# Kernel tuning notes

Measured on AMD Instinct MI355X. Metric: run time of the kernel, lower is better.

Reference implementation:

```python
import jax, jax.numpy as jnp
import numpy as np

K = 10
ALPHA = 0.1
N_NODES = 100000
N_EDGES = 5000000
HID = 16


def setup_inputs() -> dict:
    key = jax.random.key(0)
    ks = jax.random.split(key, 8)
    x = jax.random.normal(ks[0], (N_NODES, 1), dtype=jnp.float32)
    edge_index = jax.random.randint(ks[1], (2, N_EDGES), 0, N_NODES, dtype=jnp.int64)
    s = 1.0 / np.sqrt(HID)
    W1 = jax.random.normal(ks[2], (1, HID), dtype=jnp.float32)
    b1 = jax.random.normal(ks[3], (HID,), dtype=jnp.float32) * s
    W2 = jax.random.normal(ks[4], (HID, HID), dtype=jnp.float32) * s
    b2 = jax.random.normal(ks[5], (HID,), dtype=jnp.float32) * s
    W3 = jax.random.normal(ks[6], (HID, 1), dtype=jnp.float32) * s
    b3 = jax.random.normal(ks[7], (1,), dtype=jnp.float32) * s
    return {"x": x, "edge_index": edge_index, "W1": W1, "b1": b1,
            "W2": W2, "b2": b2, "W3": W3, "b3": b3}


def reference(x, edge_index, W1, b1, W2, b2, W3, b3):
    N = x.shape[0]
    # GCN normalization with self-loops (PyG APPNP default):
    # A_hat = D^{-1/2} (A + I) D^{-1/2}
    loop = jnp.arange(N, dtype=edge_index.dtype)
    src = jnp.concatenate([edge_index[0], loop])  # [E + N]
    dst = jnp.concatenate([edge_index[1], loop])
    ones = jnp.ones(src.shape[0], dtype=x.dtype)
    deg = jax.ops.segment_sum(ones, dst, num_segments=N)  # in-degree + 1
    dinv = jnp.where(deg > 0, jax.lax.rsqrt(deg), 0.0)
    norm = dinv[src] * dinv[dst]  # [E + N]

    # MLP encoder
    h = jax.nn.relu(x @ W1 + b1)
    h = jax.nn.relu(h @ W2 + b2)

    # APPNP propagation: h <- (1-alpha) * A_hat h + alpha * h0
    h0 = h
    for _ in range(K):
        msg = h[src] * norm[:, None]                         # gather + scale
        agg = jax.ops.segment_sum(msg, dst, num_segments=N)  # scatter-add
        h = (1.0 - ALPHA) * agg + ALPHA * h0

    return h @ W3 + b3
```

## Files before the change

kernel.cpp:

```cpp
#include <hip/hip_runtime.h>
#include <math.h>

#define HID 16
#define NBUCK 8
#define NSTRIPE 64
#define SLICE 11264
#define PAD 32
#define BW 12500
#define BSTEP 12500

typedef int int4v __attribute__((ext_vector_type(4)));

__global__ void partition_edges(const int* __restrict__ src, const int* __restrict__ dst,
                                int* __restrict__ scur, int* __restrict__ pairs, int E) {
    int lane = threadIdx.x & 63;
    int wib = threadIdx.x >> 6;
    int base = (blockIdx.x * 4 + wib) * 512;
    int stripe = blockIdx.x & (NSTRIPE - 1);
    unsigned long long lt = ((unsigned long long)1 << lane) - 1;

    int pk[8], bk[8], off[8];
    int wcnt[NBUCK];
#pragma unroll
    for (int b = 0; b < NBUCK; ++b) wcnt[b] = 0;

#pragma unroll
    for (int i = 0; i < 8; ++i) {
        int e = base + i * 64 + lane;
        bool valid = e < E;
        int d = valid ? dst[e] : 0;
        int s = valid ? src[e] : 0;
        int b = d / BSTEP;
        bk[i] = valid ? b : -1;
        pk[i] = ((d - b * BSTEP) << 17) | s;
#pragma unroll
        for (int bb = 0; bb < NBUCK; ++bb) {
            unsigned long long m = __ballot(valid && (b == bb));
            if (valid && b == bb) off[i] = wcnt[bb] + __popcll(m & lt);
            wcnt[bb] += __popcll(m);
        }
    }
    __shared__ int wc[4][NBUCK];
    __shared__ int wbase[4][NBUCK];
    int myc = 0;
#pragma unroll
    for (int b = 0; b < NBUCK; ++b) if (lane == b) myc = wcnt[b];
    if (lane < NBUCK) wc[wib][lane] = myc;
    __syncthreads();
    if (wib == 0 && lane < NBUCK) {
        int t0 = wc[0][lane], t1 = wc[1][lane], t2 = wc[2][lane], t3 = wc[3][lane];
        int tot = t0 + t1 + t2 + t3;
        int bb = (tot > 0) ? atomicAdd(&scur[lane * NSTRIPE + stripe], tot) : 0;
        wbase[0][lane] = bb;
        wbase[1][lane] = bb + t0;
        wbase[2][lane] = bb + t0 + t1;
        wbase[3][lane] = bb + t0 + t1 + t2;
    }
    __syncthreads();
    int mybase = (lane < NBUCK) ? wbase[wib][lane] : 0;
#pragma unroll
    for (int i = 0; i < 8; ++i) {
        if (bk[i] >= 0) {
            int b = bk[i];
            int bs = __shfl(mybase, b, 64);
            int idx = bs + off[i];
            if (idx < SLICE)
                pairs[((size_t)(b * NSTRIPE + stripe)) * SLICE + idx] = pk[i];
        }
    }
}

__global__ void count_slices(const int* __restrict__ pairs, const int* __restrict__ scur,
                             unsigned short* __restrict__ pcnt) {
    __shared__ int lcnt[BW];
    int sl = blockIdx.x;
    for (int i = threadIdx.x; i < BW; i += blockDim.x) lcnt[i] = 0;
    __syncthreads();
    int n = scur[sl];
    if (n > SLICE) n = SLICE;
    const int* seg = pairs + (size_t)sl * SLICE;
    int n4 = n >> 2;
    const int4v* seg4 = (const int4v*)seg;
    for (int q = threadIdx.x; q < n4; q += blockDim.x) {
        int4v p = seg4[q];
        atomicAdd(&lcnt[p.x >> 17], 1);
        atomicAdd(&lcnt[p.y >> 17], 1);
        atomicAdd(&lcnt[p.z >> 17], 1);
        atomicAdd(&lcnt[p.w >> 17], 1);
    }
    for (int k = (n4 << 2) + threadIdx.x; k < n; k += blockDim.x)
        atomicAdd(&lcnt[seg[k] >> 17], 1);
    __syncthreads();
    unsigned short* out = pcnt + (size_t)sl * BW;
    for (int i = threadIdx.x; i < BW; i += blockDim.x)
        out[i] = (unsigned short)lcnt[i];
}

__global__ void block_reduce(const unsigned short* __restrict__ pcnt,
                             int* __restrict__ bsum, int N) {
    int i = blockIdx.x * blockDim.x + threadIdx.x;
    int c = 0;
    if (i < N) {
        int b = i / BW;
        int loc = i - b * BW;
#pragma unroll 8
        for (int s = 0; s < NSTRIPE; ++s)
            c += pcnt[(size_t)(b * NSTRIPE + s) * BW + loc];
    }
    int v = (i < N) ? ((c + (PAD - 1)) & ~(PAD - 1)) : 0;
#pragma unroll
    for (int o = 1; o < 64; o <<= 1) v += __shfl_xor(v, o);
    __shared__ int ws[4];
    int lane = threadIdx.x & 63;
    int wid = threadIdx.x >> 6;
    if (lane == 0) ws[wid] = v;
    __syncthreads();
    if (threadIdx.x == 0) bsum[blockIdx.x] = ws[0] + ws[1] + ws[2] + ws[3];
}

__global__ void scan_bsums(int* __restrict__ bsum, int* __restrict__ row_ptr,
                           int nb, int N) {
    __shared__ int s[1024];
    int t = threadIdx.x;
    int v = (t < nb) ? bsum[t] : 0;
    s[t] = v;
    __syncthreads();
    for (int o = 1; o < 1024; o <<= 1) {
        int add = (t >= o) ? s[t - o] : 0;
        __syncthreads();
        s[t] += add;
        __syncthreads();
    }
    if (t < nb) bsum[t] = s[t] - v;
    if (t == 0) row_ptr[N] = s[1023];
}

__global__ void finalize_encode(const unsigned short* __restrict__ pcnt,
                                const int* __restrict__ bsum,
                                int* __restrict__ row_ptr, int* __restrict__ ppos,
                                float* __restrict__ w9, float* __restrict__ dinv,
                                const float* __restrict__ x, const float* __restrict__ W1,
                                const float* __restrict__ b1, const float* __restrict__ W2,
                                const float* __restrict__ b2, const float* __restrict__ W3,
                                float* __restrict__ z0, float* __restrict__ zA,
                                float* __restrict__ zB, int* __restrict__ col, int N) {
    __shared__ int sm[256];
    int t = threadIdx.x;
    int i = blockIdx.x * blockDim.x + t;
    int b = 0, loc = 0, c = 0;
    if (i < N) {
        b = i / BW;
        loc = i - b * BW;
#pragma unroll 8
        for (int s = 0; s < NSTRIPE; ++s)
            c += pcnt[(size_t)(b * NSTRIPE + s) * BW + loc];
    }
    int pc = (c + (PAD - 1)) & ~(PAD - 1);
    sm[t] = (i < N) ? pc : 0;
    __syncthreads();
    for (int o = 1; o < 256; o <<= 1) {
        int add = (t >= o) ? sm[t - o] : 0;
        __syncthreads();
        sm[t] += add;
        __syncthreads();
    }
    if (i >= N) return;
    int off = bsum[blockIdx.x] + sm[t] - pc;
    row_ptr[i] = off;
    int run = off;
#pragma unroll 8
    for (int s = 0; s < NSTRIPE; ++s) {
        ppos[(size_t)(b * NSTRIPE + s) * BW + loc] = run;
        run += pcnt[(size_t)(b * NSTRIPE + s) * BW + loc];
    }
    if (i == 0) { z0[N] = 0.0f; zA[N] = 0.0f; zB[N] = 0.0f; }
    for (int k = off + c; k < off + pc; ++k) col[k] = N;
    float deg = (float)(c + 1);
    w9[i]   = 0.9f / deg;
    float dv = rsqrtf(deg);
    dinv[i] = dv;

    float xv = x[i];
    float h1[HID];
#pragma unroll
    for (int j = 0; j < HID; ++j) h1[j] = fmaxf(xv * W1[j] + b1[j], 0.0f);
    float zacc = 0.0f;
#pragma unroll
    for (int j = 0; j < HID; ++j) {
        float acc = b2[j];
#pragma unroll
        for (int q = 0; q < HID; ++q) acc += h1[q] * W2[q * HID + j];
        zacc += fmaxf(acc, 0.0f) * W3[j];
    }
    z0[i] = dv * zacc;
}

__global__ void fill_csr3(const int* __restrict__ pairs, const int* __restrict__ scur,
                          const int* __restrict__ ppos, int* __restrict__ col) {
    __shared__ int lcur[BW];
    int b = blockIdx.x & 7;
    int s = blockIdx.x >> 3;
    int sl = b * NSTRIPE + s;
    const int* pb = ppos + (size_t)sl * BW;
    for (int i = threadIdx.x; i < BW; i += blockDim.x) lcur[i] = pb[i];
    __syncthreads();
    int n = scur[sl];
    if (n > SLICE) n = SLICE;
    const int* seg = pairs + (size_t)sl * SLICE;
    for (int k = threadIdx.x; k < n; k += blockDim.x) {
        int p = seg[k];
        int pos = atomicAdd(&lcur[p >> 17], 1);
        col[pos] = p & 0x1FFFF;
    }
}

__global__ void pack_col(const int* __restrict__ col, const int* __restrict__ row_ptr,
                         unsigned short* __restrict__ collo,
                         unsigned long long* __restrict__ colmask, int N) {
    int t = blockIdx.x * blockDim.x + threadIdx.x;
    int base = t << 6;
    if (base >= row_ptr[N]) return;
    unsigned long long m = 0;
#pragma unroll
    for (int q = 0; q < 16; ++q) {
        int4v c = *(const int4v*)(col + base + q * 4);
        unsigned long long w = (unsigned long long)(c.x & 0xFFFF)
                             | ((unsigned long long)(c.y & 0xFFFF) << 16)
                             | ((unsigned long long)(c.z & 0xFFFF) << 32)
                             | ((unsigned long long)(c.w & 0xFFFF) << 48);
        *(unsigned long long*)(collo + base + q * 4) = w;
        m |= ((unsigned long long)((c.x >> 16) & 1)) << (q * 4 + 0);
        m |= ((unsigned long long)((c.y >> 16) & 1)) << (q * 4 + 1);
        m |= ((unsigned long long)((c.z >> 16) & 1)) << (q * 4 + 2);
        m |= ((unsigned long long)((c.w >> 16) & 1)) << (q * 4 + 3);
    }
    colmask[t] = m;
}

__device__ __forceinline__ float row_sum16(const float* __restrict__ zin,
                                           const unsigned short* __restrict__ collo,
                                           const unsigned long long* __restrict__ colmask,
                                           int s, int pe, int j) {
    float a0 = 0.f, a1 = 0.f;
    for (int k = s + j * 2; k < pe; k += 32) {
        unsigned int w = *(const unsigned int*)(collo + k);
        unsigned int bits = (unsigned int)((colmask[k >> 6] >> (k & 63)) & 3ULL);
        int c0 = (int)(w & 0xFFFF)  | ((bits & 1) << 16);
        int c1 = (int)(w >> 16)     | ((bits & 2) << 15);
        a0 += zin[c0];
        a1 += zin[c1];
    }
    float acc = a0 + a1;
    acc += __shfl_xor(acc, 1, 16);
    acc += __shfl_xor(acc, 2, 16);
    acc += __shfl_xor(acc, 4, 16);
    acc += __shfl_xor(acc, 8, 16);
    return acc;
}

__device__ __forceinline__ int pin_node(int blockId, int tid) {
    int bucket = blockId & 7;
    int idx = blockId >> 3;
    return bucket * BW + idx * 16 + (tid >> 4);
}

__global__ void prop_scalar(const float* __restrict__ zin, const float* __restrict__ z0,
                            const int* __restrict__ row_ptr,
                            const unsigned short* __restrict__ collo,
                            const unsigned long long* __restrict__ colmask,
                            const float* __restrict__ w9, float* __restrict__ zout, int N) {
    int v = pin_node(blockIdx.x, threadIdx.x);
    if (v >= N) return;
    int j = threadIdx.x & 15;
    int s = row_ptr[v];
    int pe = row_ptr[v + 1];
    float acc = row_sum16(zin, collo, colmask, s, pe, j);
    if (j == 0) zout[v] = w9[v] * (acc + zin[v]) + 0.1f * z0[v];
}

__global__ void prop_last(const float* __restrict__ zin, const float* __restrict__ z0,
                          const int* __restrict__ row_ptr,
                          const unsigned short* __restrict__ collo,
                          const unsigned long long* __restrict__ colmask,
                          const float* __restrict__ w9, const float* __restrict__ dinv,
                          const float* __restrict__ b3, float* __restrict__ y, int N) {
    int v = pin_node(blockIdx.x, threadIdx.x);
    if (v >= N) return;
    int j = threadIdx.x & 15;
    int s = row_ptr[v];
    int pe = row_ptr[v + 1];
    float acc = row_sum16(zin, collo, colmask, s, pe, j);
    if (j == 0) {
        float zf = w9[v] * (acc + zin[v]) + 0.1f * z0[v];
        y[v] = zf / dinv[v] + b3[0];
    }
}

extern "C" void kernel_launch(void* const* d_in, const int* in_sizes, int n_in,
                              void* d_out, int out_size, void* d_ws, size_t ws_size,
                              hipStream_t stream) {
    const float* x  = (const float*)d_in[0];
    const int* edge = (const int*)d_in[1];
    const float* W1 = (const float*)d_in[2];
    const float* b1 = (const float*)d_in[3];
    const float* W2 = (const float*)d_in[4];
    const float* b2 = (const float*)d_in[5];
    const float* W3 = (const float*)d_in[6];
    const float* b3 = (const float*)d_in[7];
    float* y = (float*)d_out;

    const int N = in_sizes[0];
    const int E = in_sizes[1] / 2;
    const int* src = edge;
    const int* dst = edge + E;

    char* ws = (char*)d_ws;
    size_t off = 0;
    auto alloc = [&](size_t bytes) -> void* {
        void* p = ws + off;
        off += (bytes + 255) & ~(size_t)255;
        return p;
    };

    const size_t maxCol = (size_t)E + (size_t)PAD * N + 64;
    int*    row_ptr = (int*)   alloc((size_t)(N + 1) * 4);
    int*    col     = (int*)   alloc(maxCol * 4);
    unsigned short* collo = (unsigned short*)alloc(maxCol * 2);
    unsigned long long* colmask = (unsigned long long*)alloc((maxCol / 64 + 2) * 8);
    int*    pairs   = (int*)   alloc((size_t)NBUCK * NSTRIPE * SLICE * 4);
    unsigned short* pcnt = (unsigned short*)alloc((size_t)NBUCK * NSTRIPE * BW * 2);
    int*    ppos    = (int*)   alloc((size_t)NBUCK * NSTRIPE * BW * 4);
    float*  w9      = (float*) alloc((size_t)N * 4);
    float*  dinv    = (float*) alloc((size_t)N * 4);
    float*  z0f     = (float*) alloc((size_t)(N + 1) * 4);
    float*  zA      = (float*) alloc((size_t)(N + 1) * 4);
    float*  zB      = (float*) alloc((size_t)(N + 1) * 4);
    int*    bsum    = (int*)   alloc(1024 * 4);
    int*    scur    = (int*)   alloc(NBUCK * NSTRIPE * 4);

    const int nb = (N + 255) / 256;

    hipMemsetAsync(scur, 0, NBUCK * NSTRIPE * 4, stream);

    int ablocks = (E + 2047) / 2048;
    partition_edges<<<ablocks, 256, 0, stream>>>(src, dst, scur, pairs, E);
    count_slices<<<NBUCK * NSTRIPE, 256, 0, stream>>>(pairs, scur, pcnt);
    block_reduce<<<nb, 256, 0, stream>>>(pcnt, bsum, N);
    scan_bsums<<<1, 1024, 0, stream>>>(bsum, row_ptr, nb, N);
    finalize_encode<<<nb, 256, 0, stream>>>(pcnt, bsum, row_ptr, ppos, w9, dinv,
                                            x, W1, b1, W2, b2, W3, z0f, zA, zB, col, N);
    fill_csr3<<<NBUCK * NSTRIPE, 256, 0, stream>>>(pairs, scur, ppos, col);

    int pblocks = (int)((maxCol / 64 + 255) / 256);
    pack_col<<<pblocks, 256, 0, stream>>>(col, row_ptr, collo, colmask, N);

    const float* zin = z0f;
    float* zout = zA;
    int bpb = (BW + 15) / 16;
    int pgrid = 8 * bpb;
    for (int k = 0; k < 9; ++k) {
        prop_scalar<<<pgrid, 256, 0, stream>>>(zin, z0f, row_ptr, collo, colmask, w9, zout, N);
        zin = zout;
        zout = (zout == zA) ? zB : zA;
    }
    prop_last<<<pgrid, 256, 0, stream>>>(zin, z0f, row_ptr, collo, colmask, w9, dinv, b3, y, N);
}
```

Before: 450.5 us.

## Precompute per-stripe prefix offsets in a parallel stripe-scan kernel

Adds a stripe_scan kernel where 16 lanes per node cooperatively scan the 64 per-stripe counts, writing relative stripe prefixes and the node degree. block_reduce and finalize_encode then read the degree instead of each looping serially over 64 strided pcnt entries twice. fill_csr3 rebuilds absolute cursors by adding row_ptr to the relative prefix. This removes redundant serial strided reads of pcnt in two kernels, at the cost of an extra launch and an extra cdeg buffer.

```diff
diff --git a/kernel.cpp b/kernel.cpp
--- a/kernel.cpp
+++ b/kernel.cpp
@@ -96,17 +96,40 @@
         out[i] = (unsigned short)lcnt[i];
 }
 
-__global__ void block_reduce(const unsigned short* __restrict__ pcnt,
+__global__ void stripe_scan(const unsigned short* __restrict__ pcnt,
+                            int* __restrict__ pprefix, int* __restrict__ cdeg, int N) {
+    int node = blockIdx.x * 16 + (threadIdx.x >> 4);
+    if (node >= N) return;
+    int l = threadIdx.x & 15;
+    int b = node / BW;
+    int loc = node - b * BW;
+
+    int v[4];
+    int lsum = 0;
+#pragma unroll
+    for (int t = 0; t < 4; ++t) {
+        v[t] = pcnt[(size_t)(b * NSTRIPE + l * 4 + t) * BW + loc];
+        lsum += v[t];
+    }
+    int incl = lsum;
+#pragma unroll
+    for (int o = 1; o < 16; o <<= 1) {
+        int nv = __shfl(incl, l - o, 16);
+        if (l >= o) incl += nv;
+    }
+    int run = incl - lsum;
+#pragma unroll
+    for (int t = 0; t < 4; ++t) {
+        pprefix[(size_t)(b * NSTRIPE + l * 4 + t) * BW + loc] = run;
+        run += v[t];
+    }
+    if (l == 15) cdeg[node] = incl;
+}
+
+__global__ void block_reduce(const int* __restrict__ cdeg,
                              int* __restrict__ bsum, int N) {
     int i = blockIdx.x * blockDim.x + threadIdx.x;
-    int c = 0;
-    if (i < N) {
-        int b = i / BW;
-        int loc = i - b * BW;
-#pragma unroll 8
-        for (int s = 0; s < NSTRIPE; ++s)
-            c += pcnt[(size_t)(b * NSTRIPE + s) * BW + loc];
-    }
+    int c = (i < N) ? cdeg[i] : 0;
     int v = (i < N) ? ((c + (PAD - 1)) & ~(PAD - 1)) : 0;
 #pragma unroll
     for (int o = 1; o < 64; o <<= 1) v += __shfl_xor(v, o);
@@ -135,9 +158,9 @@
     if (t == 0) row_ptr[N] = s[1023];
 }
 
-__global__ void finalize_encode(const unsigned short* __restrict__ pcnt,
+__global__ void finalize_encode(const int* __restrict__ cdeg,
                                 const int* __restrict__ bsum,
-                                int* __restrict__ row_ptr, int* __restrict__ ppos,
+                                int* __restrict__ row_ptr,
                                 float* __restrict__ w9, float* __restrict__ dinv,
                                 const float* __restrict__ x, const float* __restrict__ W1,
                                 const float* __restrict__ b1, const float* __restrict__ W2,
@@ -147,14 +170,7 @@
     __shared__ int sm[256];
     int t = threadIdx.x;
     int i = blockIdx.x * blockDim.x + t;
-    int b = 0, loc = 0, c = 0;
-    if (i < N) {
-        b = i / BW;
-        loc = i - b * BW;
-#pragma unroll 8
-        for (int s = 0; s < NSTRIPE; ++s)
-            c += pcnt[(size_t)(b * NSTRIPE + s) * BW + loc];
-    }
+    int c = (i < N) ? cdeg[i] : 0;
     int pc = (c + (PAD - 1)) & ~(PAD - 1);
     sm[t] = (i < N) ? pc : 0;
     __syncthreads();
@@ -167,12 +183,6 @@
     if (i >= N) return;
     int off = bsum[blockIdx.x] + sm[t] - pc;
     row_ptr[i] = off;
-    int run = off;
-#pragma unroll 8
-    for (int s = 0; s < NSTRIPE; ++s) {
-        ppos[(size_t)(b * NSTRIPE + s) * BW + loc] = run;
-        run += pcnt[(size_t)(b * NSTRIPE + s) * BW + loc];
-    }
     if (i == 0) { z0[N] = 0.0f; zA[N] = 0.0f; zB[N] = 0.0f; }
     for (int k = off + c; k < off + pc; ++k) col[k] = N;
     float deg = (float)(c + 1);
@@ -196,13 +206,16 @@
 }
 
 __global__ void fill_csr3(const int* __restrict__ pairs, const int* __restrict__ scur,
-                          const int* __restrict__ ppos, int* __restrict__ col) {
+                          const int* __restrict__ pprefix, const int* __restrict__ row_ptr,
+                          int* __restrict__ col) {
     __shared__ int lcur[BW];
     int b = blockIdx.x & 7;
     int s = blockIdx.x >> 3;
     int sl = b * NSTRIPE + s;
-    const int* pb = ppos + (size_t)sl * BW;
-    for (int i = threadIdx.x; i < BW; i += blockDim.x) lcur[i] = pb[i];
+    int node0 = b * BW;
+    const int* pb = pprefix + (size_t)sl * BW;
+    for (int i = threadIdx.x; i < BW; i += blockDim.x)
+        lcur[i] = row_ptr[node0 + i] + pb[i];
     __syncthreads();
     int n = scur[sl];
     if (n > SLICE) n = SLICE;
@@ -329,7 +342,8 @@
     unsigned long long* colmask = (unsigned long long*)alloc((maxCol / 64 + 2) * 8);
     int*    pairs   = (int*)   alloc((size_t)NBUCK * NSTRIPE * SLICE * 4);
     unsigned short* pcnt = (unsigned short*)alloc((size_t)NBUCK * NSTRIPE * BW * 2);
-    int*    ppos    = (int*)   alloc((size_t)NBUCK * NSTRIPE * BW * 4);
+    int*    pprefix = (int*)   alloc((size_t)NBUCK * NSTRIPE * BW * 4);
+    int*    cdeg    = (int*)   alloc((size_t)N * 4);
     float*  w9      = (float*) alloc((size_t)N * 4);
     float*  dinv    = (float*) alloc((size_t)N * 4);
     float*  z0f     = (float*) alloc((size_t)(N + 1) * 4);
@@ -345,11 +359,12 @@
     int ablocks = (E + 2047) / 2048;
     partition_edges<<<ablocks, 256, 0, stream>>>(src, dst, scur, pairs, E);
     count_slices<<<NBUCK * NSTRIPE, 256, 0, stream>>>(pairs, scur, pcnt);
-    block_reduce<<<nb, 256, 0, stream>>>(pcnt, bsum, N);
+    stripe_scan<<<(N + 15) / 16, 256, 0, stream>>>(pcnt, pprefix, cdeg, N);
+    block_reduce<<<nb, 256, 0, stream>>>(cdeg, bsum, N);
     scan_bsums<<<1, 1024, 0, stream>>>(bsum, row_ptr, nb, N);
-    finalize_encode<<<nb, 256, 0, stream>>>(pcnt, bsum, row_ptr, ppos, w9, dinv,
+    finalize_encode<<<nb, 256, 0, stream>>>(cdeg, bsum, row_ptr, w9, dinv,
                                             x, W1, b1, W2, b2, W3, z0f, zA, zB, col, N);
-    fill_csr3<<<NBUCK * NSTRIPE, 256, 0, stream>>>(pairs, scur, ppos, col);
+    fill_csr3<<<NBUCK * NSTRIPE, 256, 0, stream>>>(pairs, scur, pprefix, row_ptr, col);
 
     int pblocks = (int)((maxCol / 64 + 255) / 256);
     pack_col<<<pblocks, 256, 0, stream>>>(col, row_ptr, collo, colmask, N);
```

After: 467.5 us. 3.8% more time.
